# Kernel tuning notes

Measured on AMD Instinct MI355X. Metric: run time of the kernel, lower is better.

Reference implementation:

```python
import jax, jax.numpy as jnp
import numpy as np

B, HD, H, W = 2, 4, 128, 128
KSIZE = 7
K = KSIZE * KSIZE
NSP = 9          # 3x3 superpixel candidates per pixel (hardcoded in CUDA ext)
S = 64           # number of superpixels (stride-16 grid on 128x128)


def setup_inputs() -> dict:
    key = jax.random.key(0)
    k1, k2, k3 = jax.random.split(key, 3)
    attn = jax.random.normal(k1, (B, HD, H, W, K), dtype=jnp.float32)
    sims = jax.random.uniform(k2, (B, S, H, W), dtype=jnp.float32)
    sinds = jax.random.randint(k3, (B, H, W, NSP), 0, S, dtype=jnp.int32)
    return {"attn": attn, "sims": sims, "sinds": sinds}


def _neighbor_coords(n, ks):
    # NAT-style clamped window: start = clip(i - ks//2, 0, n-ks)
    start = jnp.clip(jnp.arange(n) - ks // 2, 0, n - ks)
    return start[:, None] + jnp.arange(ks)[None, :]  # (n, ks)


def reference(attn, sims, sinds):
    eps = 1e-10
    b, hd, h, w, kk = attn.shape
    ks = int(round(kk ** 0.5))
    nsp = sinds.shape[-1]

    # stable exp of logits
    c = jnp.max(attn, axis=-1, keepdims=True)
    a = jnp.exp(attn - c)                                   # (B,HD,H,W,K)

    hj = _neighbor_coords(h, ks)                            # (H,ks)
    wj = _neighbor_coords(w, ks)                            # (W,ks)

    # p[b,h,w,s,kh,kw] = sims[b, sinds[b,h,w,s], hj[h,kh], wj[w,kw]]
    b_idx = jnp.arange(b)[:, None, None, None, None, None]
    gid = sinds[:, :, :, :, None, None]                     # (B,H,W,9,1,1)
    hj_e = hj[None, :, None, None, :, None]                 # (1,H,1,1,ks,1)
    wj_e = wj[None, None, :, None, None, :]                 # (1,1,W,1,1,ks)
    p = sims[b_idx, gid, hj_e, wj_e]                        # (B,H,W,9,ks,ks)
    p = p.reshape(b, h, w, nsp, kk).transpose(0, 3, 1, 2, 4)  # (B,9,H,W,K)

    # reweight: P(L_j = s) * exp(qk), then normalize over neighbors j
    ao = a[:, :, None, :, :, :] * p[:, None, :, :, :, :]    # (B,HD,9,H,W,K)
    ao = ao / (eps + jnp.sum(ao, axis=-1, keepdims=True))

    # pi[b,h,w,s] = P(L_i = s) = sims[b, sinds[b,h,w,s], h, w]
    h_idx = jnp.arange(h)[None, :, None, None]
    w_idx = jnp.arange(w)[None, None, :, None]
    pi = sims[jnp.arange(b)[:, None, None, None], sinds, h_idx, w_idx]  # (B,H,W,9)
    pi = pi.transpose(0, 3, 1, 2)[:, None, :, :, :, None]   # (B,1,9,H,W,1)

    return jnp.sum(pi * ao, axis=2)                         # (B,HD,H,W,K)
```

## Files before the change

kernel.cpp:

```cpp
#include <hip/hip_runtime.h>
#include <math.h>

#define BN   2
#define HDN  4
#define HN   128
#define WN   128
#define KS   7
#define KK   49
#define NSPN 9
#define SN   64
#define PPB  32
#define TPB  128
#define PROW 52

__global__ __launch_bounds__(TPB, 2) void attn_rw3(
    const float* __restrict__ attn,
    const float* __restrict__ sims,
    const int*   __restrict__ sinds,
    float*       __restrict__ out)
{
    __shared__ __align__(16) float pbuf[2][PPB * PROW];
    __shared__ int   g_lds[PPB * NSPN];
    __shared__ float pi_lds[PPB * NSPN];

    const int t    = threadIdx.x;
    const int lane = t & 63;
    const int wv   = t >> 6;
    const int bx   = blockIdx.x;
    const int wseg = bx & 3;
    const int hh   = (bx >> 2) & 127;
    const int b    = bx >> 9;
    const int ww0  = wseg * PPB;

    const int pix_c = t & 31;
    const int hd    = t >> 5;

    const float* simsB = sims + ((size_t)b << 20);
    int hs = hh - 3; hs = max(0, min(HN - KS, hs));

    float a[KK];
    {
        const size_t abase =
            ((((size_t)b * HDN + hd) * HN + hh) * WN + (ww0 + pix_c)) * (size_t)KK;
        const float* ap = attn + abase;
        #pragma unroll
        for (int j = 0; j < 12; ++j)
            __builtin_memcpy(&a[4 * j], ap + 4 * j, 16);
        a[48] = ap[48];
    }
    const int sbase = ((b * HN + hh) * WN + ww0) * NSPN;
    {
        int s0 = sinds[sbase + t];
        int s1 = sinds[sbase + t + 128];
        int s2 = (t < 32) ? sinds[sbase + t + 256] : 0;
        g_lds[t] = s0;
        g_lds[t + 128] = s1;
        if (t < 32) g_lds[t + 256] = s2;
    }
    __syncthreads();

    const int  gki  = lane / KS;
    const int  gkj  = lane - gki * KS;
    const bool gact = lane < KK;
    const int  laneoff = gact ? (gki * WN + gkj) : 0;

    float gr[16];
    auto gather_load = [&](int gv) {
        #pragma unroll
        for (int i = 0; i < 16; ++i) {
            int g   = __builtin_amdgcn_readlane(gv, i);
            int pix = wv * 16 + i;
            int ws  = ww0 + pix - 3; ws = max(0, min(WN - KS, ws));
            gr[i] = simsB[(g << 14) + hs * WN + ws + laneoff];
        }
    };
    auto gather_store = [&](int buf) {
        if (gact) {
            #pragma unroll
            for (int i = 0; i < 16; ++i)
                pbuf[buf][(wv * 16 + i) * PROW + lane] = gr[i];
        }
    };

    int gv0 = 0;
    if (lane < 16) gv0 = g_lds[(wv * 16 + lane) * NSPN];
    int pg0 = g_lds[t];
    int pg1 = g_lds[t + 128];
    int pg2 = (t < 32) ? g_lds[t + 256] : 0;

    gather_load(gv0);

    float pv0 = simsB[(pg0 << 14) + hh * WN + ww0 + (t / NSPN)];
    float pv1 = simsB[(pg1 << 14) + hh * WN + ww0 + ((t + 128) / NSPN)];
    float pv2 = 0.0f;
    if (t < 32) pv2 = simsB[(pg2 << 14) + hh * WN + ww0 + ((t + 256) / NSPN)];

    {
        float m0 = a[0], m1 = a[1], m2 = a[2], m3 = a[3];
        #pragma unroll
        for (int k = 4; k < KK; k += 4) {
            m0 = fmaxf(m0, a[k]);
            if (k + 1 < KK) m1 = fmaxf(m1, a[k + 1]);
            if (k + 2 < KK) m2 = fmaxf(m2, a[k + 2]);
            if (k + 3 < KK) m3 = fmaxf(m3, a[k + 3]);
        }
        float m = fmaxf(fmaxf(m0, m1), fmaxf(m2, m3));
        #pragma unroll
        for (int k = 0; k < KK; ++k) a[k] = __expf(a[k] - m);
    }

    pi_lds[t] = pv0;
    pi_lds[t + 128] = pv1;
    if (t < 32) pi_lds[t + 256] = pv2;
    gather_store(0);
    __syncthreads();

    float acc[KK];
    #pragma unroll
    for (int k = 0; k < KK; ++k) acc[k] = 0.0f;

    for (int sp = 0; sp < NSPN; ++sp) {
        const int buf  = sp & 1;
        const bool more = (sp + 1 < NSPN);

        int gv = 0;
        if (more && lane < 16)
            gv = g_lds[(wv * 16 + lane) * NSPN + sp + 1];
        if (more) gather_load(gv);

        float pi = pi_lds[pix_c * NSPN + sp];

        float p[KK];
        const float* prow = &pbuf[buf][pix_c * PROW];
        #pragma unroll
        for (int k4 = 0; k4 < 12; ++k4) {
            float4 v = *(const float4*)(prow + k4 * 4);
            p[k4 * 4 + 0] = v.x; p[k4 * 4 + 1] = v.y;
            p[k4 * 4 + 2] = v.z; p[k4 * 4 + 3] = v.w;
        }
        p[48] = prow[48];

        float d0 = 0.f, d1 = 0.f, d2 = 0.f, d3 = 0.f;
        #pragma unroll
        for (int k = 0; k < 48; k += 4) {
            d0 = fmaf(a[k + 0], p[k + 0], d0);
            d1 = fmaf(a[k + 1], p[k + 1], d1);
            d2 = fmaf(a[k + 2], p[k + 2], d2);
            d3 = fmaf(a[k + 3], p[k + 3], d3);
        }
        d0 = fmaf(a[48], p[48], d0);
        float d  = (d0 + d1) + (d2 + d3);

        float coef = pi * __builtin_amdgcn_rcpf(d + 1e-10f);

        #pragma unroll
        for (int k = 0; k < KK; ++k) acc[k] = fmaf(coef, p[k], acc[k]);

        if (more) {
            gather_store(buf ^ 1);
            __syncthreads();
        }
    }

    const size_t obase =
        ((((size_t)b * HDN + hd) * HN + hh) * WN + (ww0 + pix_c)) * (size_t)KK;
    #pragma unroll
    for (int k = 0; k < KK; ++k) a[k] *= acc[k];
    float* op = out + obase;
    #pragma unroll
    for (int j = 0; j < 12; ++j)
        __builtin_memcpy(op + 4 * j, &a[4 * j], 16);
    op[48] = a[48];
}

extern "C" void kernel_launch(void* const* d_in, const int* in_sizes, int n_in,
                              void* d_out, int out_size, void* d_ws, size_t ws_size,
                              hipStream_t stream) {
    const float* attn  = (const float*)d_in[0];
    const float* sims  = (const float*)d_in[1];
    const int*   sinds = (const int*)d_in[2];
    float*       outp  = (float*)d_out;

    const int blocks = BN * HN * (WN / PPB);
    attn_rw3<<<blocks, TPB, 0, stream>>>(attn, sims, sinds, outp);
}
```

Baseline: 105.4 us.

## Split superpixel loop across two wave pairs with per-wave private buffers and LDS reduction

Doubles the block to 256 threads. Two waves split the 9 superpixel candidates (4 and 5) for the same pixels, and their partial accumulators are combined through LDS before the final multiply and store. Each wave now gathers only the similarity rows its own 16 pixels need into a private double buffer, so the per-iteration block-wide barriers go away. The cost is one extra LDS reduction pass, doubled attention loads and exp work per pixel, and higher register and LDS pressure per block.

```diff
diff --git a/kernel.cpp b/kernel.cpp
--- a/kernel.cpp
+++ b/kernel.cpp
@@ -10,52 +10,58 @@
 #define NSPN 9
 #define SN   64
 #define PPB  32
-#define TPB  128
+#define TPB  256
 #define PROW 52
 
-__global__ __launch_bounds__(TPB, 2) void attn_rw3(
+__global__ __launch_bounds__(TPB, 2) void attn_rw4(
     const float* __restrict__ attn,
     const float* __restrict__ sims,
     const int*   __restrict__ sinds,
     float*       __restrict__ out)
 {
-    __shared__ __align__(16) float pbuf[2][PPB * PROW];
+    __shared__ __align__(16) float smem[4 * 2 * 16 * PROW];
     __shared__ int   g_lds[PPB * NSPN];
     __shared__ float pi_lds[PPB * NSPN];
 
     const int t    = threadIdx.x;
     const int lane = t & 63;
-    const int wv   = t >> 6;
+    const int w    = t >> 6;
+    const int pixHalf = w & 1;
+    const int sph  = w >> 1;
     const int bx   = blockIdx.x;
     const int wseg = bx & 3;
     const int hh   = (bx >> 2) & 127;
     const int b    = bx >> 9;
     const int ww0  = wseg * PPB;
 
-    const int pix_c = t & 31;
-    const int hd    = t >> 5;
+    const int pixL  = lane >> 2;
+    const int hd    = lane & 3;
+    const int pix_c = pixHalf * 16 + pixL;
 
     const float* simsB = sims + ((size_t)b << 20);
     int hs = hh - 3; hs = max(0, min(HN - KS, hs));
 
     float a[KK];
+    const size_t abase =
+        ((((size_t)b * HDN + hd) * HN + hh) * WN + (ww0 + pix_c)) * (size_t)KK;
     {
-        const size_t abase =
-            ((((size_t)b * HDN + hd) * HN + hh) * WN + (ww0 + pix_c)) * (size_t)KK;
         const float* ap = attn + abase;
         #pragma unroll
         for (int j = 0; j < 12; ++j)
             __builtin_memcpy(&a[4 * j], ap + 4 * j, 16);
         a[48] = ap[48];
     }
+
     const int sbase = ((b * HN + hh) * WN + ww0) * NSPN;
     {
         int s0 = sinds[sbase + t];
-        int s1 = sinds[sbase + t + 128];
-        int s2 = (t < 32) ? sinds[sbase + t + 256] : 0;
+        int s1 = (t < 32) ? sinds[sbase + 256 + t] : 0;
         g_lds[t] = s0;
-        g_lds[t + 128] = s1;
-        if (t < 32) g_lds[t + 256] = s2;
+        if (t < 32) g_lds[256 + t] = s1;
+        float pv0 = simsB[(s0 << 14) + hh * WN + ww0 + (t / NSPN)];
+        float pv1 = (t < 32) ? simsB[(s1 << 14) + hh * WN + ww0 + ((t + 256) / NSPN)] : 0.0f;
+        pi_lds[t] = pv0;
+        if (t < 32) pi_lds[256 + t] = pv1;
     }
     __syncthreads();
 
@@ -64,13 +70,18 @@
     const bool gact = lane < KK;
     const int  laneoff = gact ? (gki * WN + gkj) : 0;
 
+    float* pb = &smem[w * (2 * 16 * PROW)];
     float gr[16];
-    auto gather_load = [&](int gv) {
+
+    auto gather_load = [&](int sp) {
+        int gv = 0;
+        if (lane < 16)
+            gv = g_lds[(pixHalf * 16 + lane) * NSPN + sp];
         #pragma unroll
         for (int i = 0; i < 16; ++i) {
-            int g   = __builtin_amdgcn_readlane(gv, i);
-            int pix = wv * 16 + i;
-            int ws  = ww0 + pix - 3; ws = max(0, min(WN - KS, ws));
+            int g    = __builtin_amdgcn_readlane(gv, i);
+            int pixg = ww0 + pixHalf * 16 + i;
+            int ws   = pixg - 3; ws = max(0, min(WN - KS, ws));
             gr[i] = simsB[(g << 14) + hs * WN + ws + laneoff];
         }
     };
@@ -78,22 +89,14 @@
         if (gact) {
             #pragma unroll
             for (int i = 0; i < 16; ++i)
-                pbuf[buf][(wv * 16 + i) * PROW + lane] = gr[i];
+                pb[(buf * 16 + i) * PROW + lane] = gr[i];
         }
     };
 
-    int gv0 = 0;
-    if (lane < 16) gv0 = g_lds[(wv * 16 + lane) * NSPN];
-    int pg0 = g_lds[t];
-    int pg1 = g_lds[t + 128];
-    int pg2 = (t < 32) ? g_lds[t + 256] : 0;
+    const int spStart = sph ? 4 : 0;
+    const int spCnt   = sph ? 5 : 4;
 
-    gather_load(gv0);
-
-    float pv0 = simsB[(pg0 << 14) + hh * WN + ww0 + (t / NSPN)];
-    float pv1 = simsB[(pg1 << 14) + hh * WN + ww0 + ((t + 128) / NSPN)];
-    float pv2 = 0.0f;
-    if (t < 32) pv2 = simsB[(pg2 << 14) + hh * WN + ww0 + ((t + 256) / NSPN)];
+    gather_load(spStart);
 
     {
         float m0 = a[0], m1 = a[1], m2 = a[2], m3 = a[3];
@@ -109,29 +112,18 @@
         for (int k = 0; k < KK; ++k) a[k] = __expf(a[k] - m);
     }
 
-    pi_lds[t] = pv0;
-    pi_lds[t + 128] = pv1;
-    if (t < 32) pi_lds[t + 256] = pv2;
     gather_store(0);
-    __syncthreads();
 
     float acc[KK];
     #pragma unroll
     for (int k = 0; k < KK; ++k) acc[k] = 0.0f;
 
-    for (int sp = 0; sp < NSPN; ++sp) {
-        const int buf  = sp & 1;
-        const bool more = (sp + 1 < NSPN);
-
-        int gv = 0;
-        if (more && lane < 16)
-            gv = g_lds[(wv * 16 + lane) * NSPN + sp + 1];
-        if (more) gather_load(gv);
-
-        float pi = pi_lds[pix_c * NSPN + sp];
+    for (int s = 0; s < spCnt; ++s) {
+        const int buf = s & 1;
+        if (s + 1 < spCnt) gather_load(spStart + s + 1);
 
         float p[KK];
-        const float* prow = &pbuf[buf][pix_c * PROW];
+        const float* prow = pb + (buf * 16 + pixL) * PROW;
         #pragma unroll
         for (int k4 = 0; k4 < 12; ++k4) {
             float4 v = *(const float4*)(prow + k4 * 4);
@@ -149,28 +141,47 @@
             d3 = fmaf(a[k + 3], p[k + 3], d3);
         }
         d0 = fmaf(a[48], p[48], d0);
-        float d  = (d0 + d1) + (d2 + d3);
+        float d = (d0 + d1) + (d2 + d3);
 
+        float pi   = pi_lds[pix_c * NSPN + spStart + s];
         float coef = pi * __builtin_amdgcn_rcpf(d + 1e-10f);
 
         #pragma unroll
         for (int k = 0; k < KK; ++k) acc[k] = fmaf(coef, p[k], acc[k]);
 
-        if (more) {
-            gather_store(buf ^ 1);
-            __syncthreads();
-        }
+        if (s + 1 < spCnt) gather_store(buf ^ 1);
     }
 
-    const size_t obase =
-        ((((size_t)b * HDN + hd) * HN + hh) * WN + (ww0 + pix_c)) * (size_t)KK;
-    #pragma unroll
-    for (int k = 0; k < KK; ++k) a[k] *= acc[k];
-    float* op = out + obase;
-    #pragma unroll
-    for (int j = 0; j < 12; ++j)
-        __builtin_memcpy(op + 4 * j, &a[4 * j], 16);
-    op[48] = a[48];
+    __syncthreads();
+    if (sph) {
+        float* xr = &smem[(t & 127) * PROW];
+        #pragma unroll
+        for (int k4 = 0; k4 < 12; ++k4) {
+            float4 v = make_float4(acc[4 * k4], acc[4 * k4 + 1],
+                                   acc[4 * k4 + 2], acc[4 * k4 + 3]);
+            *(float4*)(xr + 4 * k4) = v;
+        }
+        xr[48] = acc[48];
+    }
+    __syncthreads();
+    if (!sph) {
+        const float* xr = &smem[t * PROW];
+        #pragma unroll
+        for (int k4 = 0; k4 < 12; ++k4) {
+            float4 v = *(const float4*)(xr + 4 * k4);
+            acc[4 * k4 + 0] += v.x; acc[4 * k4 + 1] += v.y;
+            acc[4 * k4 + 2] += v.z; acc[4 * k4 + 3] += v.w;
+        }
+        acc[48] += xr[48];
+
+        #pragma unroll
+        for (int k = 0; k < KK; ++k) a[k] *= acc[k];
+        float* op = out + abase;
+        #pragma unroll
+        for (int j = 0; j < 12; ++j)
+            __builtin_memcpy(op + 4 * j, &a[4 * j], 16);
+        op[48] = a[48];
+    }
 }
 
 extern "C" void kernel_launch(void* const* d_in, const int* in_sizes, int n_in,
@@ -182,5 +193,5 @@
     float*       outp  = (float*)d_out;
 
     const int blocks = BN * HN * (WN / PPB);
-    attn_rw3<<<blocks, TPB, 0, stream>>>(attn, sims, sinds, outp);
+    attn_rw4<<<blocks, TPB, 0, stream>>>(attn, sims, sinds, outp);
 }
```

Result: slower. 109.1 us (+3.5%).
